# Optimization experiments

Hardware: AMD Instinct MI355X
Metric: run time of the kernel (lower is better)

## Reference

```python
import jax, jax.numpy as jnp
import numpy as np

B, S, D, H, M, V, R = 2, 1024, 768, 8, 3072, 32000, 2
HD = D // H  # head_dim = qkv_dim // num_heads


def ln(x, scale, bias, eps=1e-6):
    m = jnp.mean(x, axis=-1, keepdims=True)
    v = jnp.mean(jnp.square(x - m), axis=-1, keepdims=True)
    return (x - m) * jax.lax.rsqrt(v + eps) * scale + bias


def setup_inputs() -> dict:
    key = jax.random.key(0)
    ks = jax.random.split(key, 16)
    r = lambda i, shp, s=0.02: jax.random.normal(ks[i], shp, jnp.float32) * s
    z = lambda shp: jnp.zeros(shp, jnp.float32)
    o = lambda shp: jnp.ones(shp, jnp.float32)
    return {
        'l2r_embed': jax.random.normal(ks[0], (B, S, D), jnp.float32),
        'r2l_embed': jax.random.normal(ks[1], (B, S, D), jnp.float32),
        'temb': jax.random.normal(ks[2], (B, D), jnp.float32),
        'ln_l2r_s': o((D,)), 'ln_l2r_b': z((D,)),
        'ln_r2l_s': o((D,)), 'ln_r2l_b': z((D,)),
        'Wq': r(3, (D, H, HD)), 'bq': z((H, HD)),
        'Wk': r(4, (D, H, HD)), 'bk': z((H, HD)),
        'Wv': r(5, (D, H, HD)), 'bv': z((H, HD)),
        'Wo': r(6, (H, HD, D)), 'bo': z((D,)),
        'ff_ln_s': o((D,)), 'ff_ln_b': z((D,)),
        'ff_w1': r(7, (D, M)), 'ff_b1': z((M,)),
        'ff_w2': r(8, (M, D)), 'ff_b2': z((D,)),
        'tm_w1': r(9, (D, M)), 'tm_b1': z((M,)),
        'tm_w2': r(10, (M, 4 * D)), 'tm_b2': z((4 * D,)),
        'film_w': r(11, (R, 4 * D, 2 * D)), 'film_b': z((R, 2 * D)),
        'r_w1': r(12, (R, D, M)), 'r_b1': z((R, M)),
        'r_w2': r(13, (R, M, D)), 'r_b2': z((R, D)),
        'r_ln_s': o((R, D)), 'r_ln_b': z((R, D)),
        'out_w': r(14, (D, V)), 'out_b': z((V,)),
    }


def reference(l2r_embed, r2l_embed, temb, ln_l2r_s, ln_l2r_b, ln_r2l_s, ln_r2l_b,
              Wq, bq, Wk, bk, Wv, bv, Wo, bo, ff_ln_s, ff_ln_b,
              ff_w1, ff_b1, ff_w2, ff_b2, tm_w1, tm_b1, tm_w2, tm_b2,
              film_w, film_b, r_w1, r_b1, r_w2, r_b2, r_ln_s, r_ln_b,
              out_w, out_b):
    inputs = l2r_embed + r2l_embed
    # prenorm on each direction (temb stays raw)
    l2r_n = ln(l2r_embed, ln_l2r_s, ln_l2r_b)
    r2l_n = ln(r2l_embed, ln_r2l_s, ln_r2l_b)
    # cross attention: query from sum, keys/vals from [temb, l2r, r2l]
    q = jnp.einsum('bsd,dhk->bshk', l2r_n + r2l_n, Wq) + bq
    all_e = jnp.concatenate([temb[:, None, :], l2r_n, r2l_n], axis=1)  # [B, 2S+1, D]
    k = jnp.einsum('bsd,dhk->bshk', all_e, Wk) + bk
    v = jnp.einsum('bsd,dhk->bshk', all_e, Wv) + bv
    q = q / jnp.sqrt(jnp.float32(HD))
    logits = jnp.einsum('bqhd,bkhd->bhqk', q, k)  # [B, H, S, 2S+1]
    idx = jnp.arange(S)
    l2r_mask = idx[:, None] >= idx[None, :]
    r2l_mask = idx[:, None] <= idx[None, :]
    joint = jnp.concatenate(
        [jnp.ones((S, 1), bool), l2r_mask, r2l_mask], axis=-1)[None, None]
    aw = jax.nn.softmax(
        jnp.where(joint, logits, jnp.finfo(jnp.float32).min), axis=-1)
    x = jnp.einsum('bhqk,bkhd->bqhd', aw, v)
    x = jnp.einsum('bqhd,hde->bqe', x, Wo) + bo
    x = x + inputs
    # prenorm FF block
    z = ln(x, ff_ln_s, ff_ln_b)
    z = jax.nn.relu(z @ ff_w1 + ff_b1) @ ff_w2 + ff_b2
    x = x + z
    # residual readout with FiLM conditioning
    t = jax.nn.gelu(temb @ tm_w1 + tm_b1) @ tm_w2 + tm_b2  # [B, 4D]
    for i in range(R):
        film = t @ film_w[i] + film_b[i]  # [B, 2D]
        z = jax.nn.gelu(x @ r_w1[i] + r_b1[i]) @ r_w2[i] + r_b2[i]
        x = ln(x + z, r_ln_s[i], r_ln_b[i])
        a, b = jnp.split(film[:, None, :], 2, axis=-1)
        x = a * x + b
    return x @ out_w + out_b  # [B, S, V]
```

## Files before the change

### kernel.cpp

```cpp
#include <hip/hip_runtime.h>
#include <cstdint>
#include <cstddef>

#define Bb 2
#define Ss 1024
#define Dd 768
#define Hh 8
#define HDh 96
#define Mm 3072
#define Vv 32000
#define KVr 2049

typedef __attribute__((ext_vector_type(8))) short short8v;
typedef __attribute__((ext_vector_type(4))) short short4v;
typedef __attribute__((ext_vector_type(4))) float f32x4;

#define GL16(gp, lp) __builtin_amdgcn_global_load_lds( \
    (const __attribute__((address_space(1))) void*)(gp), \
    (__attribute__((address_space(3))) void*)(lp), 16, 0, 0)

static __device__ __forceinline__ short f2bf(float f) {
  union { float f; unsigned u; } x; x.f = f;
  unsigned r = (x.u + 0x7FFFu + ((x.u >> 16) & 1u)) >> 16;
  return (short)(r & 0xFFFFu);
}

static __device__ __forceinline__ float gelu_f(float v) {
  float u = 0.7978845608028654f * (v + 0.044715f * v * v * v);
  float au = fabsf(u);
  float e = __expf(2.f * au);
  float t = 1.f - 2.f / (e + 1.f);
  return 0.5f * v * (1.f + copysignf(t, u));
}

static __device__ __forceinline__ float blk_sum(float val, float* sh) {
  #pragma unroll
  for (int off = 32; off >= 1; off >>= 1) val += __shfl_xor(val, off);
  __syncthreads();
  if ((threadIdx.x & 63) == 0) sh[threadIdx.x >> 6] = val;
  __syncthreads();
  return sh[0] + sh[1] + sh[2] + sh[3];
}

__global__ __launch_bounds__(256) void prep_kernel(
    const float* __restrict__ l2r, const float* __restrict__ r2l,
    const float* __restrict__ temb,
    const float* __restrict__ s1, const float* __restrict__ b1,
    const float* __restrict__ s2, const float* __restrict__ b2,
    float* __restrict__ inputs, short* __restrict__ qin, short* __restrict__ all_e)
{
  __shared__ float sh[4];
  const int tid = threadIdx.x;
  if (blockIdx.x >= 2048) {
    int b = blockIdx.x - 2048;
    #pragma unroll
    for (int i = 0; i < 3; ++i)
      all_e[(size_t)b * KVr * Dd + tid + i * 256] = f2bf(temb[(size_t)b * Dd + tid + i * 256]);
    return;
  }
  const int row = blockIdx.x;
  const int b = row >> 10, s = row & 1023;
  const float* ap = l2r + (size_t)row * Dd;
  const float* cp = r2l + (size_t)row * Dd;
  float a0 = ap[tid], a1 = ap[tid + 256], a2 = ap[tid + 512];
  float c0 = cp[tid], c1 = cp[tid + 256], c2 = cp[tid + 512];
  float ma = blk_sum(a0 + a1 + a2, sh) * (1.f / 768.f);
  float mc = blk_sum(c0 + c1 + c2, sh) * (1.f / 768.f);
  float va = blk_sum((a0-ma)*(a0-ma) + (a1-ma)*(a1-ma) + (a2-ma)*(a2-ma), sh) * (1.f / 768.f);
  float vc = blk_sum((c0-mc)*(c0-mc) + (c1-mc)*(c1-mc) + (c2-mc)*(c2-mc), sh) * (1.f / 768.f);
  float ia = rsqrtf(va + 1e-6f), ic = rsqrtf(vc + 1e-6f);
  size_t ro = (size_t)row * Dd;
  size_t e1 = ((size_t)b * KVr + 1 + s) * Dd;
  size_t e2 = ((size_t)b * KVr + 1 + Ss + s) * Dd;
  float av[3] = {a0, a1, a2}, cv[3] = {c0, c1, c2};
  #pragma unroll
  for (int i = 0; i < 3; ++i) {
    int c = tid + i * 256;
    float an = (av[i] - ma) * ia * s1[c] + b1[c];
    float cn = (cv[i] - mc) * ic * s2[c] + b2[c];
    inputs[ro + c] = av[i] + cv[i];
    qin[ro + c]    = f2bf(an + cn);
    all_e[e1 + c]  = f2bf(an);
    all_e[e2 + c]  = f2bf(cn);
  }
}

__global__ __launch_bounds__(256) void ln_kernel(
    const float* __restrict__ x, const float* __restrict__ sc, const float* __restrict__ bi,
    short* __restrict__ yb)
{
  __shared__ float sh[4];
  const int row = blockIdx.x, tid = threadIdx.x;
  const float* xr = x + (size_t)row * Dd;
  float v0 = xr[tid], v1 = xr[tid + 256], v2 = xr[tid + 512];
  float m = blk_sum(v0 + v1 + v2, sh) * (1.f / 768.f);
  float var = blk_sum((v0-m)*(v0-m) + (v1-m)*(v1-m) + (v2-m)*(v2-m), sh) * (1.f / 768.f);
  float inv = rsqrtf(var + 1e-6f);
  float vv[3] = {v0, v1, v2};
  #pragma unroll
  for (int i = 0; i < 3; ++i) {
    int c = tid + i * 256;
    yb[(size_t)row * Dd + c] = f2bf((vv[i] - m) * inv * sc[c] + bi[c]);
  }
}

__global__ __launch_bounds__(256) void ln_comb(
    const float* __restrict__ pk,
    const float* __restrict__ bias, const float* __restrict__ res,
    const float* __restrict__ sc, const float* __restrict__ bi,
    const float* __restrict__ film, float* __restrict__ yf, short* __restrict__ yb)
{
  __shared__ float sh[4];
  const int row = blockIdx.x, tid = threadIdx.x;
  const size_t PS = (size_t)2048 * 768;
  size_t ro = (size_t)row * Dd;
  float vv[3];
  #pragma unroll
  for (int i = 0; i < 3; ++i) {
    int c = tid + i * 256;
    float v = bias[c] + res[ro + c];
    #pragma unroll
    for (int s = 0; s < 4; ++s) v += pk[s * PS + ro + c];
    vv[i] = v;
  }
  float m = blk_sum(vv[0] + vv[1] + vv[2], sh) * (1.f / 768.f);
  float var = blk_sum((vv[0]-m)*(vv[0]-m) + (vv[1]-m)*(vv[1]-m) + (vv[2]-m)*(vv[2]-m), sh) * (1.f / 768.f);
  float inv = rsqrtf(var + 1e-6f);
  int bb = row >> 10;
  #pragma unroll
  for (int i = 0; i < 3; ++i) {
    int c = tid + i * 256;
    float o = (vv[i] - m) * inv * sc[c] + bi[c];
    o = film[(size_t)bb * 1536 + c] * o + film[(size_t)bb * 1536 + 768 + c];
    if (yf) yf[ro + c] = o;
    if (yb) yb[ro + c] = f2bf(o);
  }
}

__global__ __launch_bounds__(256) void combine_kernel(
    const float* __restrict__ pk,
    const float* __restrict__ bias, const float* __restrict__ res,
    float* __restrict__ yf, short* __restrict__ yb)
{
  const int row = blockIdx.x, tid = threadIdx.x;
  const size_t PS = (size_t)2048 * 768;
  size_t ro = (size_t)row * Dd;
  #pragma unroll
  for (int i = 0; i < 3; ++i) {
    int c = tid + i * 256;
    float v = bias[c] + res[ro + c];
    #pragma unroll
    for (int s = 0; s < 4; ++s) v += pk[s * PS + ro + c];
    yf[ro + c] = v;
    yb[ro + c] = f2bf(v);
  }
}

__global__ __launch_bounds__(256) void convT(const float* __restrict__ W, short* __restrict__ Wt,
                                             int K, int N, int ntile)
{
  __shared__ short T[64][72];
  const int bn = blockIdx.x % ntile, bk = blockIdx.x / ntile;
  const int k0 = bk * 64, n0 = bn * 64, tid = threadIdx.x;
  #pragma unroll
  for (int i = 0; i < 4; ++i) {
    int id = i * 256 + tid;
    int r = id >> 4, c4 = (id & 15) * 4;
    float4 w4 = *(const float4*)(W + (size_t)(k0 + r) * N + n0 + c4);
    T[c4 + 0][r] = f2bf(w4.x);
    T[c4 + 1][r] = f2bf(w4.y);
    T[c4 + 2][r] = f2bf(w4.z);
    T[c4 + 3][r] = f2bf(w4.w);
  }
  __syncthreads();
  #pragma unroll
  for (int i = 0; i < 4; ++i) {
    int id = i * 256 + tid;
    int n = id >> 4, k4 = (id & 15) * 4;
    short4v s = *(const short4v*)&T[n][k4];
    *(short4v*)(Wt + (size_t)(n0 + n) * K + k0 + k4) = s;
  }
}

__global__ __launch_bounds__(256) void convT4(const float* __restrict__ W0, const float* __restrict__ W1,
                                              const float* __restrict__ W2, const float* __restrict__ W3,
                                              const float* __restrict__ bk, const float* __restrict__ bv,
                                              short* __restrict__ Wt, float* __restrict__ kvb)
{
  __shared__ short T[64][72];
  const int tid = threadIdx.x;
  if (blockIdx.x == 576) {
    #pragma unroll
    for (int i = 0; i < 6; ++i) {
      int c = i * 256 + tid;
      if (c < 1536) kvb[c] = (c < 768) ? bk[c] : bv[c - 768];
    }
    return;
  }
  const int wsel = blockIdx.x / 144, rem = blockIdx.x % 144;
  const float* W = wsel == 0 ? W0 : wsel == 1 ? W1 : wsel == 2 ? W2 : W3;
  short* dst = Wt + (size_t)wsel * 768 * 768;
  const int bn = rem % 12, bk2 = rem / 12;
  const int k0 = bk2 * 64, n0 = bn * 64;
  #pragma unroll
  for (int i = 0; i < 4; ++i) {
    int id = i * 256 + tid;
    int r = id >> 4, c4 = (id & 15) * 4;
    float4 w4 = *(const float4*)(W + (size_t)(k0 + r) * 768 + n0 + c4);
    T[c4 + 0][r] = f2bf(w4.x);
    T[c4 + 1][r] = f2bf(w4.y);
    T[c4 + 2][r] = f2bf(w4.z);
    T[c4 + 3][r] = f2bf(w4.w);
  }
  __syncthreads();
  #pragma unroll
  for (int i = 0; i < 4; ++i) {
    int id = i * 256 + tid;
    int n = id >> 4, k4 = (id & 15) * 4;
    short4v s = *(const short4v*)&T[n][k4];
    *(short4v*)(dst + (size_t)(n0 + n) * 768 + k0 + k4) = s;
  }
}

template<int ACT>
__global__ __launch_bounds__(256) void gemm_bf(
    const short* __restrict__ A, const short* __restrict__ Bt,
    const float* __restrict__ bias, const float* __restrict__ res,
    float* __restrict__ C, short* __restrict__ Cbf, float* __restrict__ Cpart,
    int M, int N, int K, float scale, int mtiles, int ntiles, int ksplit)
{
  __shared__ short As[2][8192];
  __shared__ short Bs[2][8192];
  const int tid = threadIdx.x, lane = tid & 63, wv = tid >> 6;
  const int l15 = lane & 15, l4 = lane >> 4;

  const int nwg = gridDim.x;
  const int qc = nwg >> 3, rc = nwg & 7;
  const int xcd = blockIdx.x & 7, idx = blockIdx.x >> 3;
  const int wgid = (xcd < rc ? xcd * (qc + 1) : rc * (qc + 1) + (xcd - rc) * qc) + idx;
  const int by = wgid % mtiles;
  const int rest = wgid / mtiles;
  const int bx = rest % ntiles;
  const int sp = rest / ntiles;
  const int kper = K / ksplit;
  const int kbeg = sp * kper;
  const int NT = kper >> 6;

  const int m0 = by * 128, n0 = bx * 128;
  const int wm = (wv >> 1) * 64, wn = (wv & 1) * 64;
  const int r8 = lane >> 3, c8 = lane & 7;
  const int csw = ((c8 ^ r8) << 3);

  f32x4 acc[4][4];
  const f32x4 zz = {0.f, 0.f, 0.f, 0.f};
  #pragma unroll
  for (int i = 0; i < 4; ++i)
    #pragma unroll
    for (int j = 0; j < 4; ++j) acc[i][j] = zz;

  const short* Ab = A + (size_t)m0 * K + kbeg + csw;
  const short* Bp = Bt + (size_t)n0 * K + kbeg + csw;

  #pragma unroll
  for (int i = 0; i < 4; ++i) {
    int row = wv * 32 + i * 8 + r8;
    GL16(Ab + (size_t)row * K, &As[0][(wv * 4 + i) * 512]);
    GL16(Bp + (size_t)row * K, &Bs[0][(wv * 4 + i) * 512]);
  }

  int buf = 0;
  for (int t = 0; t < NT; ++t) {
    if (t + 1 < NT) {
      int k0 = (t + 1) << 6;
      #pragma unroll
      for (int i = 0; i < 4; ++i) {
        int row = wv * 32 + i * 8 + r8;
        GL16(Ab + (size_t)row * K + k0, &As[buf ^ 1][(wv * 4 + i) * 512]);
        GL16(Bp + (size_t)row * K + k0, &Bs[buf ^ 1][(wv * 4 + i) * 512]);
      }
      asm volatile("s_waitcnt vmcnt(8)" ::: "memory");
    } else {
      asm volatile("s_waitcnt vmcnt(0)" ::: "memory");
    }
    __builtin_amdgcn_s_barrier();

    short8v af[2][4], bfv[2][4];
    #pragma unroll
    for (int kk = 0; kk < 2; ++kk) {
      #pragma unroll
      for (int mi = 0; mi < 4; ++mi)
        af[kk][mi] = *(const short8v*)&As[buf][(wm + mi * 16 + l15) * 64 + ((((kk << 2) | l4) ^ (l15 & 7)) << 3)];
      #pragma unroll
      for (int ni = 0; ni < 4; ++ni)
        bfv[kk][ni] = *(const short8v*)&Bs[buf][(wn + ni * 16 + l15) * 64 + ((((kk << 2) | l4) ^ (l15 & 7)) << 3)];
    }
    __builtin_amdgcn_s_setprio(1);
    #pragma unroll
    for (int kk = 0; kk < 2; ++kk)
      #pragma unroll
      for (int mi = 0; mi < 4; ++mi)
        #pragma unroll
        for (int ni = 0; ni < 4; ++ni)
          acc[mi][ni] = __builtin_amdgcn_mfma_f32_16x16x32_bf16(af[kk][mi], bfv[kk][ni], acc[mi][ni], 0, 0, 0);
    __builtin_amdgcn_s_setprio(0);
    if (t + 1 < NT) __builtin_amdgcn_s_barrier();
    buf ^= 1;
  }

  if (Cpart) {
    float* Cp = Cpart + (size_t)sp * M * N;
    #pragma unroll
    for (int mi = 0; mi < 4; ++mi)
      #pragma unroll
      for (int r = 0; r < 4; ++r) {
        int row = m0 + wm + mi * 16 + l4 * 4 + r;
        if (row >= M) continue;
        size_t rb = (size_t)row * N;
        #pragma unroll
        for (int ni = 0; ni < 4; ++ni)
          Cp[rb + n0 + wn + ni * 16 + l15] = acc[mi][ni][r];
      }
    return;
  }

  #pragma unroll
  for (int mi = 0; mi < 4; ++mi) {
    #pragma unroll
    for (int r = 0; r < 4; ++r) {
      int row = m0 + wm + mi * 16 + l4 * 4 + r;
      if (row >= M) continue;
      size_t rb = (size_t)row * N;
      #pragma unroll
      for (int ni = 0; ni < 4; ++ni) {
        int col = n0 + wn + ni * 16 + l15;
        float val = (acc[mi][ni][r] + bias[col]) * scale;
        if (ACT == 1) val = fmaxf(val, 0.f);
        if (ACT == 2) val = gelu_f(val);
        if (res) val += res[rb + col];
        if (C)   C[rb + col] = val;
        if (Cbf) Cbf[rb + col] = f2bf(val);
      }
    }
  }
}

__global__ __launch_bounds__(512, 2) void gemm256(
    const short* __restrict__ A, const short* __restrict__ Bt,
    const float* __restrict__ bias, float* __restrict__ C,
    int M, int N, int K, int mtiles)
{
  __shared__ short As[2][8192];
  __shared__ short Bs[2][8192];
  const int tid = threadIdx.x, lane = tid & 63, wv = tid >> 6;
  const int l15 = lane & 15, l4 = lane >> 4;

  const int nwg = gridDim.x;
  const int qc = nwg >> 3, rc = nwg & 7;
  const int xcd = blockIdx.x & 7, idx = blockIdx.x >> 3;
  const int wgid = (xcd < rc ? xcd * (qc + 1) : rc * (qc + 1) + (xcd - rc) * qc) + idx;
  const int by = wgid % mtiles, bx = wgid / mtiles;
  const int m0 = by * 256, n0 = bx * 256;
  const int wm = (wv >> 2) * 128, wn = (wv & 3) * 64;

  const int srow = lane >> 2, schunk = lane & 3;
  const short* srcA = A + (size_t)(m0 + wv * 32 + srow) * K + ((schunk ^ ((srow >> 1) & 3)) << 3);
  const short* srcB = Bt + (size_t)(n0 + wv * 32 + srow) * K + ((schunk ^ ((srow >> 1) & 3)) << 3);
  const int ldsoff = wv * 1024;

  f32x4 acc[8][4];
  const f32x4 zz = {0.f, 0.f, 0.f, 0.f};
  #pragma unroll
  for (int i = 0; i < 8; ++i)
    #pragma unroll
    for (int j = 0; j < 4; ++j) acc[i][j] = zz;

  const int NT = K >> 5;
  const int rsw = (l15 >> 1) & 3;

  GL16(srcA, &As[0][ldsoff]);
  GL16(srcA + (size_t)16 * K, &As[0][ldsoff + 512]);
  GL16(srcB, &Bs[0][ldsoff]);
  GL16(srcB + (size_t)16 * K, &Bs[0][ldsoff + 512]);

  int buf = 0;
  for (int t = 0; t < NT; ++t) {
    if (t + 1 < NT) {
      int k0 = (t + 1) << 5;
      GL16(srcA + k0, &As[buf ^ 1][ldsoff]);
      GL16(srcA + (size_t)16 * K + k0, &As[buf ^ 1][ldsoff + 512]);
      GL16(srcB + k0, &Bs[buf ^ 1][ldsoff]);
      GL16(srcB + (size_t)16 * K + k0, &Bs[buf ^ 1][ldsoff + 512]);
      asm volatile("s_waitcnt vmcnt(4)" ::: "memory");
    } else {
      asm volatile("s_waitcnt vmcnt(0)" ::: "memory");
    }
    __builtin_amdgcn_s_barrier();

    short8v af[8], bfv[4];
    #pragma unroll
    for (int mi = 0; mi < 8; ++mi)
      af[mi] = *(const short8v*)&As[buf][(wm + mi * 16 + l15) * 32 + ((l4 ^ rsw) << 3)];
    #pragma unroll
    for (int ni = 0; ni < 4; ++ni)
      bfv[ni] = *(const short8v*)&Bs[buf][(wn + ni * 16 + l15) * 32 + ((l4 ^ rsw) << 3)];
    __builtin_amdgcn_s_setprio(1);
    #pragma unroll
    for (int mi = 0; mi < 8; ++mi)
      #pragma unroll
      for (int ni = 0; ni < 4; ++ni)
        acc[mi][ni] = __builtin_amdgcn_mfma_f32_16x16x32_bf16(af[mi], bfv[ni], acc[mi][ni], 0, 0, 0);
    __builtin_amdgcn_s_setprio(0);
    if (t + 1 < NT) __builtin_amdgcn_s_barrier();
    buf ^= 1;
  }

  #pragma unroll
  for (int mi = 0; mi < 8; ++mi) {
    #pragma unroll
    for (int r = 0; r < 4; ++r) {
      int row = m0 + wm + mi * 16 + l4 * 4 + r;
      size_t rb = (size_t)row * N;
      #pragma unroll
      for (int ni = 0; ni < 4; ++ni) {
        int col = n0 + wn + ni * 16 + l15;
        C[rb + col] = acc[mi][ni][r] + bias[col];
      }
    }
  }
}

__global__ __launch_bounds__(256) void attn_kernel(
    const short* __restrict__ q, const short* __restrict__ kv, short* __restrict__ o)
{
  __shared__ short Kls[64][104];
  __shared__ short Vt[96][72];
  __shared__ short Pls[4][16][72];

  const int tid = threadIdx.x, lane = tid & 63, w = tid >> 6;
  const int l15 = lane & 15, l4 = lane >> 4;
  const int qt = blockIdx.x & 15;
  const int bh = blockIdx.x >> 4;
  const int h = bh & 7, b = bh >> 3;
  const int qb = qt * 64;
  const int qw = qb + w * 16;

  short8v qf[3];
  {
    const short* qp = q + ((size_t)(b * Ss + qw + l15)) * Dd + h * HDh + l4 * 8;
    #pragma unroll
    for (int kk = 0; kk < 3; ++kk) qf[kk] = *(const short8v*)(qp + kk * 32);
  }

  const f32x4 zz = {0.f, 0.f, 0.f, 0.f};
  f32x4 Oa[6];
  #pragma unroll
  for (int fn = 0; fn < 6; ++fn) Oa[fn] = zz;
  float mrow[4], lrow[4];
  #pragma unroll
  for (int r = 0; r < 4; ++r) { mrow[r] = -3.0e38f; lrow[r] = 0.f; }

  const size_t kvbase = (size_t)b * KVr;

  for (int t = 0; t < 33; ++t) {
    int k0 = t * 64;
    bool l2r_vis = (k0 <= Ss) && (k0 - 1 <= qb + 63);
    int rmaxk = (k0 + 63 > 2 * Ss) ? 2 * Ss : (k0 + 63);
    bool r2l_vis = (k0 + 63 >= Ss + 1) && (rmaxk - (Ss + 1) >= qb);
    if (!(t == 0 || l2r_vis || r2l_vis)) continue;

    __syncthreads();
    #pragma unroll
    for (int i = 0; i < 3; ++i) {
      int id = i * 256 + tid;
      int row = id / 12, cc = (id % 12) * 8;
      const short* kp = kv + (kvbase + k0 + row) * 1536 + h * HDh + cc;
      short8v k8 = *(const short8v*)kp;
      *(short8v*)&Kls[row][cc] = k8;
      short8v v8 = *(const short8v*)(kp + 768);
      #pragma unroll
      for (int j = 0; j < 8; ++j) Vt[cc + j][row] = v8[j];
    }
    __syncthreads();

    f32x4 sc[4];
    #pragma unroll
    for (int nt = 0; nt < 4; ++nt) {
      f32x4 d = zz;
      #pragma unroll
      for (int kk = 0; kk < 3; ++kk) {
        short8v kf = *(const short8v*)&Kls[nt * 16 + l15][kk * 32 + l4 * 8];
        d = __builtin_amdgcn_mfma_f32_16x16x32_bf16(qf[kk], kf, d, 0, 0, 0);
      }
      sc[nt] = d;
    }
    float tmax[4] = {-3.0e38f, -3.0e38f, -3.0e38f, -3.0e38f};
    #pragma unroll
    for (int nt = 0; nt < 4; ++nt)
      #pragma unroll
      for (int r = 0; r < 4; ++r) {
        int qg = qw + l4 * 4 + r;
        int j = k0 + nt * 16 + l15;
        bool vis = (j == 0) ||
                   (j >= 1 && j <= Ss && (j - 1) <= qg) ||
                   (j >= Ss + 1 && j <= 2 * Ss && (j - (Ss + 1)) >= qg);
        if (!vis) sc[nt][r] = -3.0e38f;
        tmax[r] = fmaxf(tmax[r], sc[nt][r]);
      }
    #pragma unroll
    for (int r = 0; r < 4; ++r) {
      #pragma unroll
      for (int off = 8; off >= 1; off >>= 1) tmax[r] = fmaxf(tmax[r], __shfl_xor(tmax[r], off));
    }
    float scl[4];
    #pragma unroll
    for (int r = 0; r < 4; ++r) {
      float mnew = fmaxf(mrow[r], tmax[r]);
      scl[r] = __expf(mrow[r] - mnew);
      mrow[r] = mnew;
    }
    #pragma unroll
    for (int fn = 0; fn < 6; ++fn)
      #pragma unroll
      for (int r = 0; r < 4; ++r) Oa[fn][r] *= scl[r];
    float lad[4] = {0.f, 0.f, 0.f, 0.f};
    #pragma unroll
    for (int nt = 0; nt < 4; ++nt)
      #pragma unroll
      for (int r = 0; r < 4; ++r) {
        float p = __expf(sc[nt][r] - mrow[r]);
        lad[r] += p;
        Pls[w][l4 * 4 + r][nt * 16 + l15] = f2bf(p);
      }
    #pragma unroll
    for (int r = 0; r < 4; ++r) {
      #pragma unroll
      for (int off = 8; off >= 1; off >>= 1) lad[r] += __shfl_xor(lad[r], off);
      lrow[r] = lrow[r] * scl[r] + lad[r];
    }
    __syncthreads();

    short8v pf[2];
    #pragma unroll
    for (int kk = 0; kk < 2; ++kk) pf[kk] = *(const short8v*)&Pls[w][l15][kk * 32 + l4 * 8];
    #pragma unroll
    for (int fn = 0; fn < 6; ++fn) {
      #pragma unroll
      for (int kk = 0; kk < 2; ++kk) {
        short8v vf = *(const short8v*)&Vt[fn * 16 + l15][kk * 32 + l4 * 8];
        Oa[fn] = __builtin_amdgcn_mfma_f32_16x16x32_bf16(pf[kk], vf, Oa[fn], 0, 0, 0);
      }
    }
  }

  #pragma unroll
  for (int fn = 0; fn < 6; ++fn)
    #pragma unroll
    for (int r = 0; r < 4; ++r) {
      int row = qw + l4 * 4 + r;
      int col = h * HDh + fn * 16 + l15;
      o[((size_t)(b * Ss + row)) * Dd + col] = f2bf(Oa[fn][r] / lrow[r]);
    }
}

__global__ __launch_bounds__(256) void thin1(const float* __restrict__ A, const float* __restrict__ W,
                                             float* __restrict__ part, int K, int N, int nblk, int splits)
{
  __shared__ float a0s[64], a1s[64];
  const int nb = blockIdx.x % nblk, ks = blockIdx.x / nblk;
  const int kl = K / splits, kbeg = ks * kl;
  const int tid = threadIdx.x;
  for (int k = tid; k < kl; k += 256) { a0s[k] = A[kbeg + k]; a1s[k] = A[K + kbeg + k]; }
  __syncthreads();
  const int n = nb * 256 + tid;
  float acc0 = 0.f, acc1 = 0.f;
  for (int k = 0; k < kl; ++k) {
    float w = W[(size_t)(kbeg + k) * N + n];
    acc0 = fmaf(a0s[k], w, acc0);
    acc1 = fmaf(a1s[k], w, acc1);
  }
  part[(size_t)ks * 2 * N + n] = acc0;
  part[(size_t)ks * 2 * N + N + n] = acc1;
}

template<int ACT>
__global__ __launch_bounds__(256) void thin2(const float* __restrict__ part,
                                             const float* __restrict__ bias,
                                             float* __restrict__ C, int N, int splits)
{
  const int n = blockIdx.x * 256 + threadIdx.x;
  float a0 = bias[n], a1 = a0;
  for (int s = 0; s < splits; ++s) {
    a0 += part[(size_t)s * 2 * N + n];
    a1 += part[(size_t)s * 2 * N + N + n];
  }
  if (ACT == 2) { a0 = gelu_f(a0); a1 = gelu_f(a1); }
  C[n] = a0; C[N + n] = a1;
}

__global__ __launch_bounds__(256) void film1(const float* __restrict__ A,
                                             const float* __restrict__ W,
                                             float* __restrict__ part)
{
  __shared__ float a0s[48], a1s[48];
  const int nb = blockIdx.x % 12, ks = blockIdx.x / 12;
  const int kbeg = ks * 48, tid = threadIdx.x;
  for (int k = tid; k < 48; k += 256) { a0s[k] = A[kbeg + k]; a1s[k] = A[3072 + kbeg + k]; }
  __syncthreads();
  const int n = nb * 256 + tid;
  const int col = (n >= 1536) ? (n - 1536) : n;
  const float* Wp = W + ((n < 1536) ? (size_t)0 : (size_t)3072 * 1536)
                      + (size_t)kbeg * 1536 + col;
  float acc0 = 0.f, acc1 = 0.f;
  for (int k = 0; k < 48; ++k) {
    float w = Wp[(size_t)k * 1536];
    acc0 = fmaf(a0s[k], w, acc0);
    acc1 = fmaf(a1s[k], w, acc1);
  }
  part[(size_t)ks * 6144 + n] = acc0;
  part[(size_t)ks * 6144 + 3072 + n] = acc1;
}

__global__ __launch_bounds__(256) void film2(const float* __restrict__ part,
                                             const float* __restrict__ fb,
                                             float* __restrict__ f0, float* __restrict__ f1)
{
  const int n = blockIdx.x * 256 + threadIdx.x;
  float a0 = fb[n], a1 = a0;
  for (int s = 0; s < 64; ++s) {
    a0 += part[(size_t)s * 6144 + n];
    a1 += part[(size_t)s * 6144 + 3072 + n];
  }
  float* dst = (n < 1536) ? f0 : f1;
  const int c = (n >= 1536) ? (n - 1536) : n;
  dst[c] = a0;
  dst[1536 + c] = a1;
}

static void gemm_launch(int act, const short* A, const short* Bt, const float* bias,
                        const float* res, float* C, short* Cbf, float* Cpart,
                        int M, int N, int K, float scale, int ksplit, hipStream_t s)
{
  int mt = (M + 127) >> 7, nt = N >> 7;
  dim3 grid(mt * nt * ksplit), blk(256);
  if (act == 1)      gemm_bf<1><<<grid, blk, 0, s>>>(A, Bt, bias, res, C, Cbf, Cpart, M, N, K, scale, mt, nt, ksplit);
  else if (act == 2) gemm_bf<2><<<grid, blk, 0, s>>>(A, Bt, bias, res, C, Cbf, Cpart, M, N, K, scale, mt, nt, ksplit);
  else               gemm_bf<0><<<grid, blk, 0, s>>>(A, Bt, bias, res, C, Cbf, Cpart, M, N, K, scale, mt, nt, ksplit);
}

static void conv_launch(const float* W, short* Wt, int K, int N, hipStream_t s)
{
  int nt = N >> 6, kt = K >> 6;
  convT<<<dim3(nt * kt), dim3(256), 0, s>>>(W, Wt, K, N, nt);
}

static void thin_launch(int act, const float* A, const float* W, const float* bias,
                        float* C, float* part, int K, int N, hipStream_t s)
{
  int nblk = N >> 8, splits = 64;
  thin1<<<dim3(nblk * splits), dim3(256), 0, s>>>(A, W, part, K, N, nblk, splits);
  if (act == 2) thin2<2><<<dim3(nblk), dim3(256), 0, s>>>(part, bias, C, N, splits);
  else          thin2<0><<<dim3(nblk), dim3(256), 0, s>>>(part, bias, C, N, splits);
}

extern "C" void kernel_launch(void* const* d_in, const int* in_sizes, int n_in,
                              void* d_out, int out_size, void* d_ws, size_t ws_size,
                              hipStream_t stream)
{
  (void)in_sizes; (void)n_in; (void)out_size; (void)ws_size;
  const float* l2r      = (const float*)d_in[0];
  const float* r2l      = (const float*)d_in[1];
  const float* temb     = (const float*)d_in[2];
  const float* ln_l2r_s = (const float*)d_in[3];
  const float* ln_l2r_b = (const float*)d_in[4];
  const float* ln_r2l_s = (const float*)d_in[5];
  const float* ln_r2l_b = (const float*)d_in[6];
  const float* Wq = (const float*)d_in[7];
  const float* bq = (const float*)d_in[8];
  const float* Wk = (const float*)d_in[9];
  const float* bk = (const float*)d_in[10];
  const float* Wv = (const float*)d_in[11];
  const float* bv = (const float*)d_in[12];
  const float* Wo = (const float*)d_in[13];
  const float* bo = (const float*)d_in[14];
  const float* ff_ln_s = (const float*)d_in[15];
  const float* ff_ln_b = (const float*)d_in[16];
  const float* ff_w1 = (const float*)d_in[17];
  const float* ff_b1 = (const float*)d_in[18];
  const float* ff_w2 = (const float*)d_in[19];
  const float* ff_b2 = (const float*)d_in[20];
  const float* tm_w1 = (const float*)d_in[21];
  const float* tm_b1 = (const float*)d_in[22];
  const float* tm_w2 = (const float*)d_in[23];
  const float* tm_b2 = (const float*)d_in[24];
  const float* film_w = (const float*)d_in[25];
  const float* film_b = (const float*)d_in[26];
  const float* r_w1 = (const float*)d_in[27];
  const float* r_b1 = (const float*)d_in[28];
  const float* r_w2 = (const float*)d_in[29];
  const float* r_b2 = (const float*)d_in[30];
  const float* r_ln_s = (const float*)d_in[31];
  const float* r_ln_b = (const float*)d_in[32];
  const float* out_w = (const float*)d_in[33];
  const float* out_b = (const float*)d_in[34];

  uint8_t* base = (uint8_t*)d_ws;
  short* qin_bf  = (short*)(base + 0);
  short* alle_bf = (short*)(base + 3145728);
  short* qb      = (short*)(base + 9440256);
  short* kvbuf   = (short*)(base + 12585984);
  short* attn_bf = (short*)(base + 25175040);
  float* inputs  = (float*)(base + 28320768);
  float* xbuf    = (float*)(base + 34612224);
  short* xn_bf   = (short*)(base + 40903680);
  short* big_bf  = (short*)(base + 44049408);
  float* x2f     = (float*)(base + 56632320);
  short* x2bf    = (short*)(base + 62923776);
  float* x3f     = (float*)(base + 72360960);
  short* x3bf    = (short*)(base + 78652416);
  short* x4bf    = (short*)(base + 81798144);
  short* wslot   = (short*)(base + 84943872);
  uint8_t* sm    = base + 89662464;
  float* t1    = (float*)sm;
  float* tb    = (float*)(sm + 24576);
  float* f0    = (float*)(sm + 49152);
  float* f1    = (float*)(sm + 61440);
  float* kvbia = (float*)(sm + 73728);
  float* part2 = (float*)(base + 44049408);
  float* partK = (float*)(base + 0);
  short* outwT = (short*)(base + 0);

  const float qscale = 0.1020620726159658f;
  dim3 blk(256);

  thin_launch(2, temb, tm_w1, tm_b1, t1, part2, 768, 3072, stream);
  thin_launch(0, t1, tm_w2, tm_b2, tb, part2, 3072, 3072, stream);
  film1<<<dim3(12 * 64), blk, 0, stream>>>(tb, film_w, part2);
  film2<<<dim3(12), blk, 0, stream>>>(part2, film_b, f0, f1);

  prep_kernel<<<2050, blk, 0, stream>>>(l2r, r2l, temb, ln_l2r_s, ln_l2r_b, ln_r2l_s, ln_r2l_b,
                                        inputs, qin_bf, alle_bf);

  convT4<<<dim3(577), blk, 0, stream>>>(Wq, Wk, Wv, Wo, bk, bv, wslot, kvbia);

  gemm_launch(0, qin_bf, wslot, bq, nullptr, nullptr, qb, nullptr, 2048, 768, 768, qscale, 1, stream);
  gemm_launch(0, alle_bf, wslot + (size_t)768 * 768, kvbia, nullptr, nullptr, kvbuf, nullptr, 4098, 1536, 768, 1.f, 1, stream);

  attn_kernel<<<256, blk, 0, stream>>>(qb, kvbuf, attn_bf);

  gemm_launch(0, attn_bf, wslot + (size_t)3 * 768 * 768, bo, inputs, xbuf, nullptr, nullptr, 2048, 768, 768, 1.f, 1, stream);
  ln_kernel<<<2048, blk, 0, stream>>>(xbuf, ff_ln_s, ff_ln_b, xn_bf);

  conv_launch(ff_w1, wslot, 768, 3072, stream);
  gemm_launch(1, xn_bf, wslot, ff_b1, nullptr, nullptr, big_bf, nullptr, 2048, 3072, 768, 1.f, 1, stream);
  conv_launch(ff_w2, wslot, 3072, 768, stream);
  gemm_launch(0, big_bf, wslot, nullptr, nullptr, nullptr, nullptr, partK, 2048, 768, 3072, 1.f, 4, stream);
  combine_kernel<<<2048, blk, 0, stream>>>(partK, ff_b2, xbuf, x2f, x2bf);

  conv_launch(r_w1, wslot, 768, 3072, stream);
  gemm_launch(2, x2bf, wslot, r_b1, nullptr, nullptr, big_bf, nullptr, 2048, 3072, 768, 1.f, 1, stream);
  conv_launch(r_w2, wslot, 3072, 768, stream);
  gemm_launch(0, big_bf, wslot, nullptr, nullptr, nullptr, nullptr, partK, 2048, 768, 3072, 1.f, 4, stream);
  ln_comb<<<2048, blk, 0, stream>>>(partK, r_b2, x2f, r_ln_s, r_ln_b, f0, x3f, x3bf);

  conv_launch(r_w1 + (size_t)768 * 3072, wslot, 768, 3072, stream);
  gemm_launch(2, x3bf, wslot, r_b1 + 3072, nullptr, nullptr, big_bf, nullptr, 2048, 3072, 768, 1.f, 1, stream);
  conv_launch(r_w2 + (size_t)3072 * 768, wslot, 3072, 768, stream);
  gemm_launch(0, big_bf, wslot, nullptr, nullptr, nullptr, nullptr, partK, 2048, 768, 3072, 1.f, 4, stream);
  ln_comb<<<2048, blk, 0, stream>>>(partK, r_b2 + 768, x3f, r_ln_s + 768, r_ln_b + 768, f1, nullptr, x4bf);

  conv_launch(out_w, outwT, 768, 32000, stream);
  gemm256<<<dim3(8 * 125), dim3(512), 0, stream>>>(x4bf, outwT, out_b, (float*)d_out,
                                                   2048, 32000, 768, 8);
}
```

Baseline: 642.4 us.

## Halve gemm_bf K-tile for occupancy; rework gemm256 into interleaved staged pipeline

gemm_bf moves to a 32-wide K tile with half the LDS and a launch bound of 4 blocks per CU, so more workgroups can be resident. gemm256 now stages a 64-wide K tile as two 32-wide sub-slabs and splits each iteration into four MFMA phases. Global-to-LDS loads for the next buffer are interleaved between those phases, with explicit barriers and waitcnts. The aim is to hide memory latency behind MFMA work in the large output-projection GEMM. The cost is doubled LDS (128KB per block for gemm256, which may limit occupancy to one block) and many extra barriers.

```diff
diff --git a/kernel.cpp b/kernel.cpp
--- a/kernel.cpp
+++ b/kernel.cpp
@@ -223,14 +223,14 @@
 }
 
 template<int ACT>
-__global__ __launch_bounds__(256) void gemm_bf(
+__global__ __launch_bounds__(256, 4) void gemm_bf(
     const short* __restrict__ A, const short* __restrict__ Bt,
     const float* __restrict__ bias, const float* __restrict__ res,
     float* __restrict__ C, short* __restrict__ Cbf, float* __restrict__ Cpart,
     int M, int N, int K, float scale, int mtiles, int ntiles, int ksplit)
 {
-  __shared__ short As[2][8192];
-  __shared__ short Bs[2][8192];
+  __shared__ short As[2][4096];
+  __shared__ short Bs[2][4096];
   const int tid = threadIdx.x, lane = tid & 63, wv = tid >> 6;
   const int l15 = lane & 15, l4 = lane >> 4;
 
@@ -244,12 +244,17 @@
   const int sp = rest / ntiles;
   const int kper = K / ksplit;
   const int kbeg = sp * kper;
-  const int NT = kper >> 6;
+  const int NT = kper >> 5;
 
   const int m0 = by * 128, n0 = bx * 128;
   const int wm = (wv >> 1) * 64, wn = (wv & 1) * 64;
-  const int r8 = lane >> 3, c8 = lane & 7;
-  const int csw = ((c8 ^ r8) << 3);
+
+  const int srow = lane >> 2, schunk = lane & 3;
+  const int scsw = (schunk ^ ((srow >> 1) & 3)) << 3;
+  const short* sA = A + (size_t)(m0 + wv * 32 + srow) * K + kbeg + scsw;
+  const short* sB = Bt + (size_t)(n0 + wv * 32 + srow) * K + kbeg + scsw;
+  const int stBase = wv * 1024;
+  const int frsw = (l4 ^ ((l15 >> 1) & 3)) << 3;
 
   f32x4 acc[4][4];
   const f32x4 zz = {0.f, 0.f, 0.f, 0.f};
@@ -258,50 +263,38 @@
     #pragma unroll
     for (int j = 0; j < 4; ++j) acc[i][j] = zz;
 
-  const short* Ab = A + (size_t)m0 * K + kbeg + csw;
-  const short* Bp = Bt + (size_t)n0 * K + kbeg + csw;
-
-  #pragma unroll
-  for (int i = 0; i < 4; ++i) {
-    int row = wv * 32 + i * 8 + r8;
-    GL16(Ab + (size_t)row * K, &As[0][(wv * 4 + i) * 512]);
-    GL16(Bp + (size_t)row * K, &Bs[0][(wv * 4 + i) * 512]);
-  }
+  GL16(sA, &As[0][stBase]);
+  GL16(sA + (size_t)16 * K, &As[0][stBase + 512]);
+  GL16(sB, &Bs[0][stBase]);
+  GL16(sB + (size_t)16 * K, &Bs[0][stBase + 512]);
 
   int buf = 0;
   for (int t = 0; t < NT; ++t) {
     if (t + 1 < NT) {
-      int k0 = (t + 1) << 6;
-      #pragma unroll
-      for (int i = 0; i < 4; ++i) {
-        int row = wv * 32 + i * 8 + r8;
-        GL16(Ab + (size_t)row * K + k0, &As[buf ^ 1][(wv * 4 + i) * 512]);
-        GL16(Bp + (size_t)row * K + k0, &Bs[buf ^ 1][(wv * 4 + i) * 512]);
-      }
-      asm volatile("s_waitcnt vmcnt(8)" ::: "memory");
+      int k0 = (t + 1) << 5;
+      GL16(sA + k0, &As[buf ^ 1][stBase]);
+      GL16(sA + (size_t)16 * K + k0, &As[buf ^ 1][stBase + 512]);
+      GL16(sB + k0, &Bs[buf ^ 1][stBase]);
+      GL16(sB + (size_t)16 * K + k0, &Bs[buf ^ 1][stBase + 512]);
+      asm volatile("s_waitcnt vmcnt(4)" ::: "memory");
     } else {
       asm volatile("s_waitcnt vmcnt(0)" ::: "memory");
     }
     __builtin_amdgcn_s_barrier();
 
-    short8v af[2][4], bfv[2][4];
-    #pragma unroll
-    for (int kk = 0; kk < 2; ++kk) {
-      #pragma unroll
-      for (int mi = 0; mi < 4; ++mi)
-        af[kk][mi] = *(const short8v*)&As[buf][(wm + mi * 16 + l15) * 64 + ((((kk << 2) | l4) ^ (l15 & 7)) << 3)];
+    short8v af[4], bfv[4];
+    #pragma unroll
+    for (int mi = 0; mi < 4; ++mi)
+      af[mi] = *(const short8v*)&As[buf][(wm + mi * 16 + l15) * 32 + frsw];
+    #pragma unroll
+    for (int ni = 0; ni < 4; ++ni)
+      bfv[ni] = *(const short8v*)&Bs[buf][(wn + ni * 16 + l15) * 32 + frsw];
+    __builtin_amdgcn_s_setprio(1);
+    #pragma unroll
+    for (int mi = 0; mi < 4; ++mi)
       #pragma unroll
       for (int ni = 0; ni < 4; ++ni)
-        bfv[kk][ni] = *(const short8v*)&Bs[buf][(wn + ni * 16 + l15) * 64 + ((((kk << 2) | l4) ^ (l15 & 7)) << 3)];
-    }
-    __builtin_amdgcn_s_setprio(1);
-    #pragma unroll
-    for (int kk = 0; kk < 2; ++kk)
-      #pragma unroll
-      for (int mi = 0; mi < 4; ++mi)
-        #pragma unroll
-        for (int ni = 0; ni < 4; ++ni)
-          acc[mi][ni] = __builtin_amdgcn_mfma_f32_16x16x32_bf16(af[kk][mi], bfv[kk][ni], acc[mi][ni], 0, 0, 0);
+        acc[mi][ni] = __builtin_amdgcn_mfma_f32_16x16x32_bf16(af[mi], bfv[ni], acc[mi][ni], 0, 0, 0);
     __builtin_amdgcn_s_setprio(0);
     if (t + 1 < NT) __builtin_amdgcn_s_barrier();
     buf ^= 1;
@@ -349,8 +342,8 @@
     const float* __restrict__ bias, float* __restrict__ C,
     int M, int N, int K, int mtiles)
 {
-  __shared__ short As[2][8192];
-  __shared__ short Bs[2][8192];
+  __shared__ short As[2][16384];
+  __shared__ short Bs[2][16384];
   const int tid = threadIdx.x, lane = tid & 63, wv = tid >> 6;
   const int l15 = lane & 15, l4 = lane >> 4;
 
@@ -363,9 +356,20 @@
   const int wm = (wv >> 2) * 128, wn = (wv & 3) * 64;
 
   const int srow = lane >> 2, schunk = lane & 3;
-  const short* srcA = A + (size_t)(m0 + wv * 32 + srow) * K + ((schunk ^ ((srow >> 1) & 3)) << 3);
-  const short* srcB = Bt + (size_t)(n0 + wv * 32 + srow) * K + ((schunk ^ ((srow >> 1) & 3)) << 3);
-  const int ldsoff = wv * 1024;
+  const int scsw = (schunk ^ ((srow >> 1) & 3)) << 3;
+  const short* sA = A + (size_t)(m0 + wv * 16 + srow) * K + scsw;
+  const short* sB = Bt + (size_t)(n0 + wv * 16 + srow) * K + scsw;
+  const int stBase = wv * 512;
+  const int frsw = (l4 ^ ((l15 >> 1) & 3)) << 3;
+
+  #define STG_A(b, kk, ko) do { \
+    GL16(sA + (ko) + (kk) * 32,                  &As[b][(kk) * 8192 + stBase]); \
+    GL16(sA + (size_t)128 * K + (ko) + (kk) * 32, &As[b][(kk) * 8192 + 4096 + stBase]); } while (0)
+  #define STG_B(b, kk, ko) do { \
+    GL16(sB + (ko) + (kk) * 32,                  &Bs[b][(kk) * 8192 + stBase]); \
+    GL16(sB + (size_t)128 * K + (ko) + (kk) * 32, &Bs[b][(kk) * 8192 + 4096 + stBase]); } while (0)
+  #define ARD(b, kk, row) (*(const short8v*)&As[b][(kk) * 8192 + (row) * 32 + frsw])
+  #define BRD(b, kk, row) (*(const short8v*)&Bs[b][(kk) * 8192 + (row) * 32 + frsw])
 
   f32x4 acc[8][4];
   const f32x4 zz = {0.f, 0.f, 0.f, 0.f};
@@ -374,43 +378,85 @@
     #pragma unroll
     for (int j = 0; j < 4; ++j) acc[i][j] = zz;
 
-  const int NT = K >> 5;
-  const int rsw = (l15 >> 1) & 3;
-
-  GL16(srcA, &As[0][ldsoff]);
-  GL16(srcA + (size_t)16 * K, &As[0][ldsoff + 512]);
-  GL16(srcB, &Bs[0][ldsoff]);
-  GL16(srcB + (size_t)16 * K, &Bs[0][ldsoff + 512]);
+  const int NT = K >> 6;
+
+  STG_A(0, 0, 0); STG_B(0, 0, 0); STG_A(0, 1, 0); STG_B(0, 1, 0);
+  asm volatile("s_waitcnt vmcnt(4)" ::: "memory");
+  __builtin_amdgcn_s_barrier();
 
   int buf = 0;
   for (int t = 0; t < NT; ++t) {
-    if (t + 1 < NT) {
-      int k0 = (t + 1) << 5;
-      GL16(srcA + k0, &As[buf ^ 1][ldsoff]);
-      GL16(srcA + (size_t)16 * K + k0, &As[buf ^ 1][ldsoff + 512]);
-      GL16(srcB + k0, &Bs[buf ^ 1][ldsoff]);
-      GL16(srcB + (size_t)16 * K + k0, &Bs[buf ^ 1][ldsoff + 512]);
-      asm volatile("s_waitcnt vmcnt(4)" ::: "memory");
-    } else {
-      asm volatile("s_waitcnt vmcnt(0)" ::: "memory");
-    }
+    const bool pf = (t + 1 < NT);
+    const int k1 = (t + 1) << 6;
+    short8v af[4], bfv[4];
+
+    #pragma unroll
+    for (int mi = 0; mi < 4; ++mi) af[mi] = ARD(buf, 0, wm + mi * 16 + l15);
+    #pragma unroll
+    for (int ni = 0; ni < 4; ++ni) bfv[ni] = BRD(buf, 0, wn + ni * 16 + l15);
+    if (pf) STG_A(buf ^ 1, 0, k1);
     __builtin_amdgcn_s_barrier();
-
-    short8v af[8], bfv[4];
-    #pragma unroll
-    for (int mi = 0; mi < 8; ++mi)
-      af[mi] = *(const short8v*)&As[buf][(wm + mi * 16 + l15) * 32 + ((l4 ^ rsw) << 3)];
-    #pragma unroll
-    for (int ni = 0; ni < 4; ++ni)
-      bfv[ni] = *(const short8v*)&Bs[buf][(wn + ni * 16 + l15) * 32 + ((l4 ^ rsw) << 3)];
+    asm volatile("s_waitcnt lgkmcnt(0)" ::: "memory");
+    __builtin_amdgcn_sched_barrier(0);
     __builtin_amdgcn_s_setprio(1);
     #pragma unroll
-    for (int mi = 0; mi < 8; ++mi)
+    for (int mi = 0; mi < 4; ++mi)
       #pragma unroll
       for (int ni = 0; ni < 4; ++ni)
         acc[mi][ni] = __builtin_amdgcn_mfma_f32_16x16x32_bf16(af[mi], bfv[ni], acc[mi][ni], 0, 0, 0);
     __builtin_amdgcn_s_setprio(0);
-    if (t + 1 < NT) __builtin_amdgcn_s_barrier();
+    __builtin_amdgcn_s_barrier();
+
+    #pragma unroll
+    for (int mi = 0; mi < 4; ++mi) af[mi] = ARD(buf, 0, wm + 64 + mi * 16 + l15);
+    if (pf) STG_B(buf ^ 1, 0, k1);
+    __builtin_amdgcn_s_barrier();
+    asm volatile("s_waitcnt lgkmcnt(0)" ::: "memory");
+    __builtin_amdgcn_sched_barrier(0);
+    __builtin_amdgcn_s_setprio(1);
+    #pragma unroll
+    for (int mi = 0; mi < 4; ++mi)
+      #pragma unroll
+      for (int ni = 0; ni < 4; ++ni)
+        acc[4 + mi][ni] = __builtin_amdgcn_mfma_f32_16x16x32_bf16(af[mi], bfv[ni], acc[4 + mi][ni], 0, 0, 0);
+    __builtin_amdgcn_s_setprio(0);
+    if (pf) asm volatile("s_waitcnt vmcnt(4)" ::: "memory");
+    else    asm volatile("s_waitcnt vmcnt(0)" ::: "memory");
+    __builtin_amdgcn_s_barrier();
+
+    #pragma unroll
+    for (int mi = 0; mi < 4; ++mi) af[mi] = ARD(buf, 1, wm + mi * 16 + l15);
+    #pragma unroll
+    for (int ni = 0; ni < 4; ++ni) bfv[ni] = BRD(buf, 1, wn + ni * 16 + l15);
+    if (pf) STG_A(buf ^ 1, 1, k1);
+    __builtin_amdgcn_s_barrier();
+    asm volatile("s_waitcnt lgkmcnt(0)" ::: "memory");
+    __builtin_amdgcn_sched_barrier(0);
+    __builtin_amdgcn_s_setprio(1);
+    #pragma unroll
+    for (int mi = 0; mi < 4; ++mi)
+      #pragma unroll
+      for (int ni = 0; ni < 4; ++ni)
+        acc[mi][ni] = __builtin_amdgcn_mfma_f32_16x16x32_bf16(af[mi], bfv[ni], acc[mi][ni], 0, 0, 0);
+    __builtin_amdgcn_s_setprio(0);
+    __builtin_amdgcn_s_barrier();
+
+    #pragma unroll
+    for (int mi = 0; mi < 4; ++mi) af[mi] = ARD(buf, 1, wm + 64 + mi * 16 + l15);
+    if (pf) STG_B(buf ^ 1, 1, k1);
+    __builtin_amdgcn_s_barrier();
+    asm volatile("s_waitcnt lgkmcnt(0)" ::: "memory");
+    __builtin_amdgcn_sched_barrier(0);
+    __builtin_amdgcn_s_setprio(1);
+    #pragma unroll
+    for (int mi = 0; mi < 4; ++mi)
+      #pragma unroll
+      for (int ni = 0; ni < 4; ++ni)
+        acc[4 + mi][ni] = __builtin_amdgcn_mfma_f32_16x16x32_bf16(af[mi], bfv[ni], acc[4 + mi][ni], 0, 0, 0);
+    __builtin_amdgcn_s_setprio(0);
+    if (pf) asm volatile("s_waitcnt vmcnt(4)" ::: "memory");
+    __builtin_amdgcn_s_barrier();
+
     buf ^= 1;
   }
 
@@ -427,6 +473,10 @@
       }
     }
   }
+  #undef STG_A
+  #undef STG_B
+  #undef ARD
+  #undef BRD
 }
 
 __global__ __launch_bounds__(256) void attn_kernel(
```

New measurement: 645.3 us. Within noise of the previous version (+0.4%).
